# Performance work log

Measured on AMD Instinct MI355X. Metric: run time of the kernel, lower is better.

Reference implementation:

```python
import jax, jax.numpy as jnp
from jax import lax
import numpy as np

B, L = 256, 4096
H, RL, RH = 128, 2, 32   # num_hiddens, residual layers, residual hiddens
K, D = 512, 64           # codebook size, embedding dim
CC = 0.25                # commitment cost


def conv1d(x, w, b=None, stride=1, pad=0, circular=False):
    # x: (N,C,L), w: (O,I,k)
    if circular and pad > 0:
        x = jnp.pad(x, ((0, 0), (0, 0), (pad, pad)), mode='wrap')
        pad = 0
    y = lax.conv_general_dilated(x, w, (stride,), [(pad, pad)],
                                 dimension_numbers=('NCH', 'OIH', 'NCH'))
    return y if b is None else y + b[None, :, None]


def convt1d(x, w, b):
    # PyTorch ConvTranspose1d(k=4, s=2, p=1); w: (I,O,4). out_len = 2*L.
    wt = jnp.flip(jnp.swapaxes(w, 0, 1), -1)  # (O,I,4)
    y = lax.conv_general_dilated(x, wt, (1,), [(2, 2)], lhs_dilation=(2,),
                                 dimension_numbers=('NCH', 'OIH', 'NCH'))
    return y + b[None, :, None]


def res_stack(x, w1s, w2s):
    for i in range(w1s.shape[0]):
        h = conv1d(jax.nn.relu(x), w1s[i], None, 1, 1, circular=True)
        h = conv1d(jax.nn.relu(h), w2s[i], None, 1, 0)
        x = x + h
    return jax.nn.relu(x)


def setup_inputs() -> dict:
    key = jax.random.key(0)
    ks = iter(jax.random.split(key, 64))

    def w(*shape):
        fan_in = int(np.prod(shape[1:]))
        return jax.random.normal(next(ks), shape, jnp.float32) / np.sqrt(fan_in)

    def bias(n):
        return jax.random.uniform(next(ks), (n,), jnp.float32, -0.05, 0.05)

    inp = {'x': jax.random.normal(next(ks), (B, 1, L), jnp.float32)}
    # Encoder
    inp['enc_c1_w'] = w(H // 2, 1, 4);      inp['enc_c1_b'] = bias(H // 2)
    inp['enc_c2_w'] = w(H, H // 2, 4);      inp['enc_c2_b'] = bias(H)
    inp['enc_c3_w'] = w(H, H, 4);           inp['enc_c3_b'] = bias(H)
    inp['enc_c4_w'] = w(H, H, 4);           inp['enc_c4_b'] = bias(H)
    inp['enc_cf_w'] = w(H, H, 3);           inp['enc_cf_b'] = bias(H)
    inp['enc_res_w1'] = w(RL, RH, H, 3)
    inp['enc_res_w2'] = w(RL, H, RH, 1)
    # pre-VQ 1x1 conv
    inp['prevq_w'] = w(D, H, 1);            inp['prevq_b'] = bias(D)
    # codebook: uniform(-1/K, 1/K) as in source
    inp['emb'] = jax.random.uniform(next(ks), (K, D), jnp.float32, -1.0 / K, 1.0 / K)
    # Decoder
    inp['dec_init_w'] = w(H, D, 3);         inp['dec_init_b'] = bias(H)
    inp['dec_res_w1'] = w(RL, RH, H, 3)
    inp['dec_res_w2'] = w(RL, H, RH, 1)
    inp['ct0_w'] = w(H, H, 4);              inp['ct0_b'] = bias(H)
    inp['ct1_w'] = w(H, H, 4);              inp['ct1_b'] = bias(H)
    inp['ct2_w'] = w(H, H // 2, 4);         inp['ct2_b'] = bias(H // 2)
    inp['ct3_w'] = w(H // 2, 1, 4);         inp['ct3_b'] = bias(1)
    return inp


def _forward(x, enc_c1_w, enc_c1_b, enc_c2_w, enc_c2_b, enc_c3_w, enc_c3_b,
             enc_c4_w, enc_c4_b, enc_cf_w, enc_cf_b, enc_res_w1, enc_res_w2,
             prevq_w, prevq_b, emb, dec_init_w, dec_init_b, dec_res_w1,
             dec_res_w2, ct0_w, ct0_b, ct1_w, ct1_b, ct2_w, ct2_b, ct3_w, ct3_b):
    sg = lax.stop_gradient
    relu = jax.nn.relu
    # ---- Encoder (circular padding) ----
    z = relu(conv1d(x, enc_c1_w, enc_c1_b, 2, 1, circular=True))
    z = relu(conv1d(z, enc_c2_w, enc_c2_b, 2, 1, circular=True))
    z = relu(conv1d(z, enc_c3_w, enc_c3_b, 2, 1, circular=True))
    z = relu(conv1d(z, enc_c4_w, enc_c4_b, 2, 1, circular=True))
    z = conv1d(z, enc_cf_w, enc_cf_b, 1, 1, circular=True)
    z = res_stack(z, enc_res_w1, enc_res_w2)
    z = conv1d(z, prevq_w, prevq_b, 1, 0)        # (B, D, T)
    # ---- Vector quantizer ----
    z_t = jnp.transpose(z, (0, 2, 1))            # (B, T, D)
    flat = z_t.reshape(-1, D)                    # (BT, D)
    dist = (jnp.sum(flat ** 2, axis=1, keepdims=True)
            + jnp.sum(emb ** 2, axis=1)
            - 2.0 * flat @ emb.T)                # (BT, K)
    idx = jnp.argmin(dist, axis=1)               # (BT,)
    enc = jax.nn.one_hot(idx, K, dtype=flat.dtype)
    q = (enc @ emb).reshape(z_t.shape)           # (B, T, D)
    e_loss = jnp.mean((sg(q) - z_t) ** 2)
    q_loss = jnp.mean((q - sg(z_t)) ** 2)
    loss = q_loss + CC * e_loss
    q_st = z_t + sg(q - z_t)                     # straight-through
    avg = jnp.mean(enc, axis=0)
    perplexity = jnp.exp(-jnp.sum(avg * jnp.log(avg + 1e-10)))
    quantized = jnp.transpose(q_st, (0, 2, 1))   # (B, D, T)
    # ---- Decoder ----
    h = conv1d(quantized, dec_init_w, dec_init_b, 1, 1)
    h = res_stack(h, dec_res_w1, dec_res_w2)
    h = relu(convt1d(h, ct0_w, ct0_b))
    h = relu(convt1d(h, ct1_w, ct1_b))
    h = relu(convt1d(h, ct2_w, ct2_b))
    x_recon = convt1d(h, ct3_w, ct3_b)           # (B, 1, L)
    return loss, x_recon, perplexity


def reference(x, enc_c1_w, enc_c1_b, enc_c2_w, enc_c2_b, enc_c3_w, enc_c3_b,
              enc_c4_w, enc_c4_b, enc_cf_w, enc_cf_b, enc_res_w1, enc_res_w2,
              prevq_w, prevq_b, emb, dec_init_w, dec_init_b, dec_res_w1,
              dec_res_w2, ct0_w, ct0_b, ct1_w, ct1_b, ct2_w, ct2_b, ct3_w, ct3_b):
    return _forward(x, enc_c1_w, enc_c1_b, enc_c2_w, enc_c2_b, enc_c3_w,
                    enc_c3_b, enc_c4_w, enc_c4_b, enc_cf_w, enc_cf_b,
                    enc_res_w1, enc_res_w2, prevq_w, prevq_b, emb,
                    dec_init_w, dec_init_b, dec_res_w1, dec_res_w2,
                    ct0_w, ct0_b, ct1_w, ct1_b, ct2_w, ct2_b, ct3_w, ct3_b)
```

## Files before the change

### kernel.cpp

```cpp
#include <hip/hip_runtime.h>

#define DEVI __device__ __forceinline__

typedef __bf16 bf16x8 __attribute__((ext_vector_type(8)));
typedef float f32x4 __attribute__((ext_vector_type(4)));

DEVI ushort f2b(float f) {
  uint b = __float_as_uint(f);
  uint r = (b + 0x7FFFu + ((b >> 16) & 1u)) >> 16;
  return (ushort)r;
}
DEVI float b2f(ushort u) { return __uint_as_float(((uint)u) << 16); }

struct PrepArgs {
  int nw;
  int tot[20];
  const float* src[20];
  ushort* dst[20];
  int ci[20], co[20], sco[20], sci[20], sk[20];
};

__global__ __launch_bounds__(256)
void prep_all(PrepArgs a, int total) {
  int i = blockIdx.x * 256 + threadIdx.x;
  if (i >= total) return;
  int w = 0;
  while (i >= a.tot[w]) { i -= a.tot[w]; ++w; }
  const int li = i;
  const int CI = a.ci[w];
  int ciX = i % CI;
  int rest = i / CI;
  int coX = rest % a.co[w];
  int k = rest / a.co[w];
  a.dst[w][li] = f2b(a.src[w][coX * a.sco[w] + ciX * a.sci[w] + k * a.sk[w]]);
}

__global__ __launch_bounds__(256)
void enc1_bf(const float* __restrict__ x, const float* __restrict__ w1,
             const float* __restrict__ b1, ushort* __restrict__ out) {
  int i = blockIdx.x * 256 + threadIdx.x;
  int t = i & 2047, n = i >> 11;
  const float* xb = x + ((size_t)n << 12);
  int p = 2 * t - 1;
  float x0 = xb[(p + 4096) & 4095];
  float x1 = xb[(p + 4097) & 4095];
  float x2 = xb[(p + 4098) & 4095];
  float x3 = xb[(p + 4099) & 4095];
  uint ow[32];
  #pragma unroll
  for (int c2 = 0; c2 < 32; ++c2) {
    float4 wa = *reinterpret_cast<const float4*>(w1 + 8 * c2);
    float4 wb = *reinterpret_cast<const float4*>(w1 + 8 * c2 + 4);
    float s0 = fmaf(wa.x, x0, fmaf(wa.y, x1, fmaf(wa.z, x2, fmaf(wa.w, x3, b1[2 * c2]))));
    float s1 = fmaf(wb.x, x0, fmaf(wb.y, x1, fmaf(wb.z, x2, fmaf(wb.w, x3, b1[2 * c2 + 1]))));
    ow[c2] = (uint)f2b(fmaxf(s0, 0.0f)) | ((uint)f2b(fmaxf(s1, 0.0f)) << 16);
  }
  uint4* op = reinterpret_cast<uint4*>(out + ((size_t)i << 6));
  #pragma unroll
  for (int q = 0; q < 8; ++q)
    op[q] = uint4{ow[4 * q], ow[4 * q + 1], ow[4 * q + 2], ow[4 * q + 3]};
}

template<int CI, int CO, int K, int S, bool CIRC, bool GATHER, int NT, int WAVES_CO>
__global__ __launch_bounds__(256)
void conv_mfma(const ushort* __restrict__ in, const ushort* __restrict__ wb,
               const float* __restrict__ bias, const ushort* __restrict__ resid,
               ushort* __restrict__ out, const int* __restrict__ gidx,
               int Tin, int in_relu, int out_relu) {
  constexpr int PAD = (K > 1) ? 1 : 0;
  constexpr int TT = NT * 16;
  constexpr int SPAN = S * (TT - 1) + K;
  constexpr int CIG = CI / 8;
  constexpr int COT = CO / 16;
  constexpr int WCOT = COT / WAVES_CO;
  constexpr int WAVES_T = 4 / WAVES_CO;
  constexpr int WTT = NT / WAVES_T;
  constexpr int KSH = (S == 2) ? 1 : 0;
  static_assert(CI % 32 == 0 && COT % WAVES_CO == 0 && NT % WAVES_T == 0, "");

  __shared__ __align__(16) ushort xs[SPAN * CI];

  const int Tout = Tin / S;
  const int tilesPerB = Tout / TT;
  const int n = blockIdx.x / tilesPerB;
  const int t0 = (blockIdx.x % tilesPerB) * TT;
  const int tid = threadIdx.x;
  const int wid = tid >> 6, lane = tid & 63;
  const int l15 = lane & 15, l4 = lane >> 4;

  const int t_in0 = S * t0 - PAD;
  const ushort* inb = GATHER ? in : in + (size_t)n * Tin * CI;
  for (int i = tid; i < SPAN * CIG; i += 256) {
    int t = i / CIG, g = i - (i / CIG) * CIG;
    int tg = t_in0 + t;
    uint4 v;
    if (CIRC) {
      tg = (tg < 0) ? tg + Tin : (tg >= Tin ? tg - Tin : tg);
      v = *reinterpret_cast<const uint4*>(inb + (size_t)tg * CI + g * 8);
    } else if (GATHER) {
      if ((unsigned)tg < (unsigned)Tin) {
        int id = gidx[n * Tin + tg];
        v = *reinterpret_cast<const uint4*>(inb + (size_t)id * CI + g * 8);
      } else
        v = uint4{0, 0, 0, 0};
    } else {
      if ((unsigned)tg < (unsigned)Tin)
        v = *reinterpret_cast<const uint4*>(inb + (size_t)tg * CI + g * 8);
      else
        v = uint4{0, 0, 0, 0};
    }
    if (in_relu) {
      ushort* pv = reinterpret_cast<ushort*>(&v);
      #pragma unroll
      for (int e = 0; e < 8; ++e) pv[e] = (pv[e] & 0x8000) ? 0 : pv[e];
    }
    *reinterpret_cast<uint4*>(&xs[t * CI + ((g ^ ((t >> KSH) & (CIG - 1))) * 8)]) = v;
  }
  __syncthreads();

  const int wco = wid % WAVES_CO;
  const int wt = wid / WAVES_CO;
  const int co_base = wco * WCOT * 16;
  const int t_base = wt * WTT * 16;

  f32x4 acc[WTT][WCOT] = {};

  for (int cc = 0; cc < CI / 32; ++cc) {
    bf16x8 bk[K][WCOT];
    #pragma unroll
    for (int k = 0; k < K; ++k)
      #pragma unroll
      for (int c = 0; c < WCOT; ++c)
        bk[k][c] = __builtin_bit_cast(bf16x8, *reinterpret_cast<const uint4*>(
            wb + (size_t)((k * CO + co_base + c * 16 + l15)) * CI + cc * 32 + l4 * 8));
    #pragma unroll
    for (int k = 0; k < K; ++k) {
      #pragma unroll
      for (int tt2 = 0; tt2 < WTT; ++tt2) {
        int trow = S * (t_base + tt2 * 16 + l15) + k;
        int g = cc * 4 + l4;
        bf16x8 afr = __builtin_bit_cast(bf16x8, *reinterpret_cast<const uint4*>(
            &xs[trow * CI + ((g ^ ((trow >> KSH) & (CIG - 1))) * 8)]));
        #pragma unroll
        for (int c = 0; c < WCOT; ++c)
          acc[tt2][c] = __builtin_amdgcn_mfma_f32_16x16x32_bf16(afr, bk[k][c], acc[tt2][c], 0, 0, 0);
      }
    }
  }

  float bv[WCOT];
  #pragma unroll
  for (int c = 0; c < WCOT; ++c)
    bv[c] = bias ? bias[co_base + c * 16 + l15] : 0.0f;
  ushort* outb = out + (size_t)n * Tout * CO;
  const ushort* resb = resid ? resid + (size_t)n * Tout * CO : nullptr;
  #pragma unroll
  for (int tt2 = 0; tt2 < WTT; ++tt2)
    #pragma unroll
    for (int c = 0; c < WCOT; ++c)
      #pragma unroll
      for (int r = 0; r < 4; ++r) {
        int t = t0 + t_base + tt2 * 16 + 4 * l4 + r;
        int co = co_base + c * 16 + l15;
        float v = acc[tt2][c][r] + bv[c];
        if (resb) v += b2f(resb[(size_t)t * CO + co]);
        if (out_relu) v = fmaxf(v, 0.0f);
        outb[(size_t)t * CO + co] = f2b(v);
      }
}

__global__ __launch_bounds__(256)
void res_mfma(const ushort* __restrict__ in, const ushort* __restrict__ wb1,
              const ushort* __restrict__ wb2, ushort* __restrict__ out) {
  constexpr int CI = 128, CIG = 16;
  constexpr int TT = 64, SPAN = 66, Tin = 256;
  __shared__ __align__(16) ushort xs[SPAN * CI];
  __shared__ __align__(16) ushort hs[TT][40];
  const int n = blockIdx.x >> 2;
  const int t0 = (blockIdx.x & 3) * TT;
  const int tid = threadIdx.x;
  const int wid = tid >> 6, lane = tid & 63;
  const int l15 = lane & 15, l4 = lane >> 4;
  const int t_in0 = t0 - 1;
  const ushort* inb = in + (size_t)n * Tin * CI;

  for (int i = tid; i < SPAN * CIG; i += 256) {
    int t = i >> 4, g = i & 15;
    int tg = t_in0 + t;
    tg = (tg < 0) ? tg + Tin : (tg >= Tin ? tg - Tin : tg);
    uint4 v = *reinterpret_cast<const uint4*>(inb + (size_t)tg * CI + g * 8);
    ushort* pv = reinterpret_cast<ushort*>(&v);
    #pragma unroll
    for (int e = 0; e < 8; ++e) pv[e] = (pv[e] & 0x8000) ? 0 : pv[e];
    *reinterpret_cast<uint4*>(&xs[t * CI + ((g ^ (t & 15)) * 8)]) = v;
  }
  __syncthreads();

  {
    f32x4 acc[2] = {};
    for (int cc = 0; cc < 4; ++cc)
      #pragma unroll
      for (int k = 0; k < 3; ++k) {
        bf16x8 bfr[2];
        #pragma unroll
        for (int c = 0; c < 2; ++c)
          bfr[c] = __builtin_bit_cast(bf16x8, *reinterpret_cast<const uint4*>(
              wb1 + (size_t)((k * 32 + c * 16 + l15)) * CI + cc * 32 + l4 * 8));
        int trow = wid * 16 + l15 + k;
        int g = cc * 4 + l4;
        bf16x8 afr = __builtin_bit_cast(bf16x8, *reinterpret_cast<const uint4*>(
            &xs[trow * CI + ((g ^ (trow & 15)) * 8)]));
        acc[0] = __builtin_amdgcn_mfma_f32_16x16x32_bf16(afr, bfr[0], acc[0], 0, 0, 0);
        acc[1] = __builtin_amdgcn_mfma_f32_16x16x32_bf16(afr, bfr[1], acc[1], 0, 0, 0);
      }
    #pragma unroll
    for (int c = 0; c < 2; ++c)
      #pragma unroll
      for (int r = 0; r < 4; ++r) {
        float v = acc[c][r];
        hs[wid * 16 + l4 * 4 + r][c * 16 + l15] = (v > 0.0f) ? f2b(v) : (ushort)0;
      }
  }
  __syncthreads();

  {
    bf16x8 afr = *reinterpret_cast<const bf16x8*>(&hs[wid * 16 + l15][l4 * 8]);
    f32x4 acc[8];
    #pragma unroll
    for (int c = 0; c < 8; ++c) {
      bf16x8 bfr = __builtin_bit_cast(bf16x8, *reinterpret_cast<const uint4*>(
          wb2 + (size_t)(c * 16 + l15) * 32 + l4 * 8));
      f32x4 z = {};
      acc[c] = __builtin_amdgcn_mfma_f32_16x16x32_bf16(afr, bfr, z, 0, 0, 0);
    }
    ushort* outb = out + (size_t)n * Tin * CI;
    #pragma unroll
    for (int c = 0; c < 8; ++c)
      #pragma unroll
      for (int r = 0; r < 4; ++r) {
        int t = t0 + wid * 16 + l4 * 4 + r;
        int co = c * 16 + l15;
        float v = acc[c][r] + b2f(inb[(size_t)t * CI + co]);
        outb[(size_t)t * CI + co] = f2b(v);
      }
  }
}

template<int CO>
__global__ __launch_bounds__(256)
void convt_mfma(const ushort* __restrict__ in, const ushort* __restrict__ wb,
                const float* __restrict__ bias, ushort* __restrict__ out,
                int Tin, int in_relu, int out_relu) {
  constexpr int CI = 128, CIG = 16;
  constexpr int NT = 4, TT = 64;
  constexpr int SPAN = TT + 2;
  constexpr int COT = CO / 16;
  constexpr int WCOT = (COT + 3) / 4;
  constexpr int WAVES_CO = COT / WCOT;
  constexpr int WTT = NT;

  __shared__ __align__(16) ushort xs[SPAN * CI];

  const int Tout = 2 * Tin;
  const int tilesPerB = Tin / TT;
  const int n = blockIdx.x / tilesPerB;
  const int tp0 = (blockIdx.x % tilesPerB) * TT;
  const int tid = threadIdx.x;
  const int wid = tid >> 6, lane = tid & 63;
  const int l15 = lane & 15, l4 = lane >> 4;

  const int t_in0 = tp0 - 1;
  const ushort* inb = in + (size_t)n * Tin * CI;
  for (int i = tid; i < SPAN * CIG; i += 256) {
    int t = i >> 4, g = i & 15;
    int tg = t_in0 + t;
    uint4 v;
    if ((unsigned)tg < (unsigned)Tin)
      v = *reinterpret_cast<const uint4*>(inb + (size_t)tg * CI + g * 8);
    else
      v = uint4{0, 0, 0, 0};
    if (in_relu) {
      ushort* pv = reinterpret_cast<ushort*>(&v);
      #pragma unroll
      for (int e = 0; e < 8; ++e) pv[e] = (pv[e] & 0x8000) ? 0 : pv[e];
    }
    *reinterpret_cast<uint4*>(&xs[t * CI + ((g ^ (t & 15)) * 8)]) = v;
  }
  __syncthreads();

  const int wco = wid % WAVES_CO;
  const int co_base = wco * WCOT * 16;

  f32x4 accE[WTT][WCOT] = {};
  f32x4 accO[WTT][WCOT] = {};

  for (int cc = 0; cc < 4; ++cc) {
    bf16x8 bk[4][WCOT];
    #pragma unroll
    for (int k = 0; k < 4; ++k)
      #pragma unroll
      for (int c = 0; c < WCOT; ++c)
        bk[k][c] = __builtin_bit_cast(bf16x8, *reinterpret_cast<const uint4*>(
            wb + (size_t)((k * CO + co_base + c * 16 + l15)) * CI + cc * 32 + l4 * 8));
    #pragma unroll
    for (int tt2 = 0; tt2 < WTT; ++tt2) {
      int lt = tt2 * 16 + l15 + 1;
      int g = cc * 4 + l4;
      bf16x8 a0 = __builtin_bit_cast(bf16x8, *reinterpret_cast<const uint4*>(
          &xs[lt * CI + ((g ^ (lt & 15)) * 8)]));
      bf16x8 am = __builtin_bit_cast(bf16x8, *reinterpret_cast<const uint4*>(
          &xs[(lt - 1) * CI + ((g ^ ((lt - 1) & 15)) * 8)]));
      bf16x8 ap = __builtin_bit_cast(bf16x8, *reinterpret_cast<const uint4*>(
          &xs[(lt + 1) * CI + ((g ^ ((lt + 1) & 15)) * 8)]));
      #pragma unroll
      for (int c = 0; c < WCOT; ++c) {
        accE[tt2][c] = __builtin_amdgcn_mfma_f32_16x16x32_bf16(a0, bk[1][c], accE[tt2][c], 0, 0, 0);
        accE[tt2][c] = __builtin_amdgcn_mfma_f32_16x16x32_bf16(am, bk[3][c], accE[tt2][c], 0, 0, 0);
        accO[tt2][c] = __builtin_amdgcn_mfma_f32_16x16x32_bf16(ap, bk[0][c], accO[tt2][c], 0, 0, 0);
        accO[tt2][c] = __builtin_amdgcn_mfma_f32_16x16x32_bf16(a0, bk[2][c], accO[tt2][c], 0, 0, 0);
      }
    }
  }

  float bv[WCOT];
  #pragma unroll
  for (int c = 0; c < WCOT; ++c) bv[c] = bias[co_base + c * 16 + l15];
  ushort* outb = out + (size_t)n * Tout * CO;
  #pragma unroll
  for (int tt2 = 0; tt2 < WTT; ++tt2)
    #pragma unroll
    for (int c = 0; c < WCOT; ++c)
      #pragma unroll
      for (int r = 0; r < 4; ++r) {
        int tp = tp0 + tt2 * 16 + 4 * l4 + r;
        int co = co_base + c * 16 + l15;
        float vE = accE[tt2][c][r] + bv[c];
        float vO = accO[tt2][c][r] + bv[c];
        if (out_relu) { vE = fmaxf(vE, 0.0f); vO = fmaxf(vO, 0.0f); }
        outb[(size_t)(2 * tp) * CO + co] = f2b(vE);
        outb[(size_t)(2 * tp + 1) * CO + co] = f2b(vO);
      }
}

__global__ __launch_bounds__(256)
void ct23_mfma(const ushort* __restrict__ in, const ushort* __restrict__ wb,
               const float* __restrict__ bias, const float* __restrict__ w3,
               const float* __restrict__ b3, float* __restrict__ out) {
  constexpr int CI = 128, CO = 64, CIG = 16;
  constexpr int TT = 64, SPAN = 66, Tin = 1024;
  __shared__ __align__(16) ushort xs[SPAN * CI];
  __shared__ __align__(16) ushort ys[130 * 64];

  const int n = blockIdx.x >> 4;
  const int tp0 = (blockIdx.x & 15) * TT;
  const int tid = threadIdx.x;
  const int wid = tid >> 6, lane = tid & 63;
  const int l15 = lane & 15, l4 = lane >> 4;
  const int t_in0 = tp0 - 1;
  const ushort* inb = in + (size_t)n * Tin * CI;

  for (int i = tid; i < SPAN * CIG; i += 256) {
    int t = i >> 4, g = i & 15;
    int tg = t_in0 + t;
    uint4 v;
    if ((unsigned)tg < (unsigned)Tin)
      v = *reinterpret_cast<const uint4*>(inb + (size_t)tg * CI + g * 8);
    else
      v = uint4{0, 0, 0, 0};
    *reinterpret_cast<uint4*>(&xs[t * CI + ((g ^ (t & 15)) * 8)]) = v;
  }
  __syncthreads();

  const int co_base = wid * 16;
  f32x4 accE[4] = {}, accO[4] = {};
  f32x4 hO = {}, hE = {};

  for (int cc = 0; cc < 4; ++cc) {
    bf16x8 bk[4];
    #pragma unroll
    for (int k = 0; k < 4; ++k)
      bk[k] = __builtin_bit_cast(bf16x8, *reinterpret_cast<const uint4*>(
          wb + (size_t)((k * CO + co_base + l15)) * CI + cc * 32 + l4 * 8));
    const int g = cc * 4 + l4;
    auto rd = [&](int lt) -> bf16x8 {
      return __builtin_bit_cast(bf16x8, *reinterpret_cast<const uint4*>(
          &xs[lt * CI + ((g ^ (lt & 15)) * 8)]));
    };
    #pragma unroll
    for (int tt2 = 0; tt2 < 4; ++tt2) {
      int lt = tt2 * 16 + l15 + 1;
      bf16x8 a0 = rd(lt), am = rd(lt - 1), ap = rd(lt + 1);
      accE[tt2] = __builtin_amdgcn_mfma_f32_16x16x32_bf16(a0, bk[1], accE[tt2], 0, 0, 0);
      accE[tt2] = __builtin_amdgcn_mfma_f32_16x16x32_bf16(am, bk[3], accE[tt2], 0, 0, 0);
      accO[tt2] = __builtin_amdgcn_mfma_f32_16x16x32_bf16(ap, bk[0], accO[tt2], 0, 0, 0);
      accO[tt2] = __builtin_amdgcn_mfma_f32_16x16x32_bf16(a0, bk[2], accO[tt2], 0, 0, 0);
    }
    bf16x8 h0 = rd(0), h1 = rd(1), h64 = rd(64), h65 = rd(65);
    hO = __builtin_amdgcn_mfma_f32_16x16x32_bf16(h1, bk[0], hO, 0, 0, 0);
    hO = __builtin_amdgcn_mfma_f32_16x16x32_bf16(h0, bk[2], hO, 0, 0, 0);
    hE = __builtin_amdgcn_mfma_f32_16x16x32_bf16(h65, bk[1], hE, 0, 0, 0);
    hE = __builtin_amdgcn_mfma_f32_16x16x32_bf16(h64, bk[3], hE, 0, 0, 0);
  }

  const float bv = bias[co_base + l15];
  auto ywr = [&](int j, int co, float v) {
    int g = co >> 3, e = co & 7;
    ys[j * 64 + ((g ^ (j & 7)) * 8) + e] = f2b(fmaxf(v, 0.0f));
  };
  #pragma unroll
  for (int tt2 = 0; tt2 < 4; ++tt2)
    #pragma unroll
    for (int r = 0; r < 4; ++r) {
      int m = tt2 * 16 + 4 * l4 + r;
      ywr(2 * m + 1, co_base + l15, accE[tt2][r] + bv);
      ywr(2 * m + 2, co_base + l15, accO[tt2][r] + bv);
    }
  if (l4 == 0) {
    float vO = (tp0 == 0) ? -1.0f : hO[0] + bv;
    float vE = (tp0 + TT == Tin) ? -1.0f : hE[0] + bv;
    ywr(0, co_base + l15, vO);
    ywr(129, co_base + l15, vE);
  }
  __syncthreads();

  const int o = 4 * tp0 + tid;
  const int odd = o & 1;
  const int ga = odd ? ((o + 1) >> 1) : (o >> 1);
  const int gb = odd ? ((o - 1) >> 1) : (o / 2 - 1);
  const int ka = odd ? 0 : 1;
  const int kb = odd ? 2 : 3;
  const int la = ga - (2 * tp0 - 1), lb = gb - (2 * tp0 - 1);
  float s = b3[0];
  #pragma unroll
  for (int g = 0; g < 8; ++g) {
    uint4 va = *reinterpret_cast<const uint4*>(&ys[la * 64 + ((g ^ (la & 7)) * 8)]);
    uint4 vb = *reinterpret_cast<const uint4*>(&ys[lb * 64 + ((g ^ (lb & 7)) * 8)]);
    const ushort* pa = reinterpret_cast<const ushort*>(&va);
    const ushort* pb = reinterpret_cast<const ushort*>(&vb);
    #pragma unroll
    for (int e = 0; e < 8; ++e) {
      int ci = g * 8 + e;
      s = fmaf(w3[ci * 4 + ka], b2f(pa[e]), s);
      s = fmaf(w3[ci * 4 + kb], b2f(pb[e]), s);
    }
  }
  out[(size_t)n * 4096 + o] = s;
}

__global__ void ee_kernel(const float* __restrict__ emb, float* __restrict__ ee) {
  int c = blockIdx.x * 256 + threadIdx.x;
  if (c >= 512) return;
  float s = 0.0f;
  #pragma unroll
  for (int d = 0; d < 64; ++d) { float v = emb[c * 64 + d]; s = fmaf(v, v, s); }
  ee[c] = s;
}

__global__ __launch_bounds__(256)
void vq_mfma(const ushort* __restrict__ zt, const ushort* __restrict__ embb,
             const float* __restrict__ ee, int* __restrict__ idx,
             int* __restrict__ hist, float* __restrict__ loss_accum) {
  __shared__ __align__(16) ushort es[512 * 64];
  __shared__ float eel[512];
  __shared__ int lhist[512];
  const int tid = threadIdx.x;
  const int wid = tid >> 6, lane = tid & 63;
  const int l15 = lane & 15, l4 = lane >> 4;

  for (int i = tid; i < 512 * 8; i += 256) {
    int c = i >> 3, g = i & 7;
    reinterpret_cast<uint4*>(es)[c * 8 + (g ^ (c & 7))] =
        reinterpret_cast<const uint4*>(embb)[i];
  }
  for (int i = tid; i < 512; i += 256) { eel[i] = ee[i]; lhist[i] = 0; }
  __syncthreads();

  const int rb = blockIdx.x * 256 + wid * 64;
  bf16x8 bz[4][2];
  float zz[4], best[4];
  int bi[4];
  #pragma unroll
  for (int rt = 0; rt < 4; ++rt) {
    const int r = rb + rt * 16 + l15;
    uint4 v0 = *reinterpret_cast<const uint4*>(zt + (size_t)r * 64 + l4 * 8);
    uint4 v1 = *reinterpret_cast<const uint4*>(zt + (size_t)r * 64 + 32 + l4 * 8);
    bz[rt][0] = __builtin_bit_cast(bf16x8, v0);
    bz[rt][1] = __builtin_bit_cast(bf16x8, v1);
    float s = 0.0f;
    const ushort* p0 = reinterpret_cast<const ushort*>(&v0);
    const ushort* p1 = reinterpret_cast<const ushort*>(&v1);
    #pragma unroll
    for (int e = 0; e < 8; ++e) {
      float f0 = b2f(p0[e]), f1 = b2f(p1[e]);
      s = fmaf(f0, f0, fmaf(f1, f1, s));
    }
    s += __shfl_xor(s, 16);
    s += __shfl_xor(s, 32);
    zz[rt] = s;
    best[rt] = 3.4e38f;
    bi[rt] = 0;
  }

  for (int ct = 0; ct < 32; ++ct) {
    const int c = ct * 16 + l15;
    bf16x8 a0 = __builtin_bit_cast(bf16x8, reinterpret_cast<const uint4*>(es)[
        c * 8 + (l4 ^ (c & 7))]);
    bf16x8 a1 = __builtin_bit_cast(bf16x8, reinterpret_cast<const uint4*>(es)[
        c * 8 + ((4 | l4) ^ (c & 7))]);
    #pragma unroll
    for (int rt = 0; rt < 4; ++rt) {
      f32x4 acc = {};
      acc = __builtin_amdgcn_mfma_f32_16x16x32_bf16(a0, bz[rt][0], acc, 0, 0, 0);
      acc = __builtin_amdgcn_mfma_f32_16x16x32_bf16(a1, bz[rt][1], acc, 0, 0, 0);
      #pragma unroll
      for (int rr = 0; rr < 4; ++rr) {
        int code = ct * 16 + l4 * 4 + rr;
        float d = eel[code] - 2.0f * acc[rr];
        if (d < best[rt] || (d == best[rt] && code < bi[rt])) { best[rt] = d; bi[rt] = code; }
      }
    }
  }
  float vsum = 0.0f;
  #pragma unroll
  for (int rt = 0; rt < 4; ++rt) {
    #pragma unroll
    for (int m = 16; m <= 32; m <<= 1) {
      float ob = __shfl_xor(best[rt], m);
      int oi = __shfl_xor(bi[rt], m);
      if (ob < best[rt] || (ob == best[rt] && oi < bi[rt])) { best[rt] = ob; bi[rt] = oi; }
    }
    if (l4 == 0) {
      idx[rb + rt * 16 + l15] = bi[rt];
      atomicAdd(&lhist[bi[rt]], 1);
      vsum += zz[rt] + best[rt];
    }
  }
  #pragma unroll
  for (int m = 1; m < 64; m <<= 1) vsum += __shfl_xor(vsum, m);
  if (lane == 0) atomicAdd(loss_accum, vsum);
  __syncthreads();
  for (int i = tid; i < 512; i += 256)
    if (lhist[i]) atomicAdd(&hist[i], lhist[i]);
}

__global__ __launch_bounds__(512)
void finalize(const int* __restrict__ hist, const float* __restrict__ loss_accum,
              float* __restrict__ out) {
  __shared__ float red[8];
  int tid = threadIdx.x;
  float avg = (float)hist[tid] * (1.0f / 65536.0f);
  float v = avg * logf(avg + 1e-10f);
  for (int off = 32; off > 0; off >>= 1) v += __shfl_down(v, off);
  if ((tid & 63) == 0) red[tid >> 6] = v;
  __syncthreads();
  if (tid == 0) {
    float s = 0.0f;
    for (int i = 0; i < 8; ++i) s += red[i];
    out[1048577] = expf(-s);
    out[0] = 1.25f * loss_accum[0] * (1.0f / (65536.0f * 64.0f));
  }
}

extern "C" void kernel_launch(void* const* d_in, const int* in_sizes, int n_in,
                              void* d_out, int out_size, void* d_ws, size_t ws_size,
                              hipStream_t stream) {
  (void)in_sizes; (void)n_in; (void)out_size; (void)ws_size;
  const float* x    = (const float*)d_in[0];
  const float* c1w  = (const float*)d_in[1];
  const float* c1b  = (const float*)d_in[2];
  const float* c2w  = (const float*)d_in[3];
  const float* c2b  = (const float*)d_in[4];
  const float* c3w  = (const float*)d_in[5];
  const float* c3b  = (const float*)d_in[6];
  const float* c4w  = (const float*)d_in[7];
  const float* c4b  = (const float*)d_in[8];
  const float* cfw  = (const float*)d_in[9];
  const float* cfb  = (const float*)d_in[10];
  const float* erw1 = (const float*)d_in[11];
  const float* erw2 = (const float*)d_in[12];
  const float* pqw  = (const float*)d_in[13];
  const float* pqb  = (const float*)d_in[14];
  const float* emb  = (const float*)d_in[15];
  const float* diw  = (const float*)d_in[16];
  const float* dib  = (const float*)d_in[17];
  const float* drw1 = (const float*)d_in[18];
  const float* drw2 = (const float*)d_in[19];
  const float* t0w  = (const float*)d_in[20];
  const float* t0b  = (const float*)d_in[21];
  const float* t1w  = (const float*)d_in[22];
  const float* t1b  = (const float*)d_in[23];
  const float* t2w  = (const float*)d_in[24];
  const float* t2b  = (const float*)d_in[25];
  const float* t3w  = (const float*)d_in[26];
  const float* t3b  = (const float*)d_in[27];

  char* wsb = (char*)d_ws;
  ushort* R0 = (ushort*)wsb;
  ushort* R1 = (ushort*)(wsb + 67108864);
  ushort* R2 = (ushort*)(wsb + 134217728);
  ushort* R3 = (ushort*)(wsb + 0);
  ushort* R4 = (ushort*)(wsb + 16777216);
  ushort* R6 = (ushort*)(wsb + 37748736);
  ushort* WPu = (ushort*)(wsb + 167772160);
  ushort* wb_e2 = WPu + 0;
  ushort* wb_e3 = WPu + 32768;
  ushort* wb_e4 = WPu + 98304;
  ushort* wb_cf = WPu + 163840;
  ushort* wb_r1a = WPu + 212992;
  ushort* wb_r1b = WPu + 225280;
  ushort* wb_r2a = WPu + 237568;
  ushort* wb_r2b = WPu + 241664;
  ushort* wb_pq = WPu + 245760;
  ushort* wb_di = WPu + 253952;
  ushort* wb_d1a = WPu + 278528;
  ushort* wb_d1b = WPu + 290816;
  ushort* wb_d2a = WPu + 303104;
  ushort* wb_d2b = WPu + 307200;
  ushort* wb_t0 = WPu + 311296;
  ushort* wb_t1 = WPu + 376832;
  ushort* wb_t2 = WPu + 442368;
  ushort* wb_emb = WPu + 475136;
  char* fp = wsb + 167772160 + 1048576;
  float* eeb   = (float*)fp;
  int*   idxb  = (int*)(fp + 2048);
  int*   histb = (int*)(fp + 2048 + 262144);
  float* lossb = (float*)(fp + 2048 + 262144 + 2048);
  float* outp  = (float*)d_out;

  hipMemsetAsync(histb, 0, 512 * sizeof(int), stream);
  hipMemsetAsync(lossb, 0, sizeof(float), stream);

  PrepArgs pa{};
  int nw = 0, total = 0;
  auto addw = [&](const float* src, ushort* dst, int CO, int CI, int K,
                  int sco, int sci, int sk) {
    pa.tot[nw] = K * CO * CI; pa.src[nw] = src; pa.dst[nw] = dst;
    pa.ci[nw] = CI; pa.co[nw] = CO; pa.sco[nw] = sco; pa.sci[nw] = sci; pa.sk[nw] = sk;
    total += pa.tot[nw]; ++nw;
  };
  addw(c2w, wb_e2, 128, 64, 4, 256, 4, 1);
  addw(c3w, wb_e3, 128, 128, 4, 512, 4, 1);
  addw(c4w, wb_e4, 128, 128, 4, 512, 4, 1);
  addw(cfw, wb_cf, 128, 128, 3, 384, 3, 1);
  addw(erw1, wb_r1a, 32, 128, 3, 384, 3, 1);
  addw(erw1 + 12288, wb_r1b, 32, 128, 3, 384, 3, 1);
  addw(erw2, wb_r2a, 128, 32, 1, 32, 1, 1);
  addw(erw2 + 4096, wb_r2b, 128, 32, 1, 32, 1, 1);
  addw(pqw, wb_pq, 64, 128, 1, 128, 1, 1);
  addw(diw, wb_di, 128, 64, 3, 192, 3, 1);
  addw(drw1, wb_d1a, 32, 128, 3, 384, 3, 1);
  addw(drw1 + 12288, wb_d1b, 32, 128, 3, 384, 3, 1);
  addw(drw2, wb_d2a, 128, 32, 1, 32, 1, 1);
  addw(drw2 + 4096, wb_d2b, 128, 32, 1, 32, 1, 1);
  addw(t0w, wb_t0, 128, 128, 4, 4, 512, 1);
  addw(t1w, wb_t1, 128, 128, 4, 4, 512, 1);
  addw(t2w, wb_t2, 64, 128, 4, 4, 256, 1);
  addw(emb, wb_emb, 512, 64, 1, 64, 1, 1);
  pa.nw = nw;
  prep_all<<<(total + 255) / 256, 256, 0, stream>>>(pa, total);
  ee_kernel<<<2, 256, 0, stream>>>(emb, eeb);

  enc1_bf<<<2048, 256, 0, stream>>>(x, c1w, c1b, R0);
  conv_mfma<64, 128, 4, 2, true, false, 4, 4><<<4096, 256, 0, stream>>>(R0, wb_e2, c2b, nullptr, R1, nullptr, 2048, 0, 1);
  conv_mfma<128, 128, 4, 2, true, false, 4, 4><<<2048, 256, 0, stream>>>(R1, wb_e3, c3b, nullptr, R2, nullptr, 1024, 0, 1);
  conv_mfma<128, 128, 4, 2, true, false, 4, 4><<<1024, 256, 0, stream>>>(R2, wb_e4, c4b, nullptr, R3, nullptr, 512, 0, 1);
  conv_mfma<128, 128, 3, 1, true, false, 8, 2><<<512, 256, 0, stream>>>(R3, wb_cf, cfb, nullptr, R4, nullptr, 256, 0, 0);
  res_mfma<<<1024, 256, 0, stream>>>(R4, wb_r1a, wb_r2a, R3);
  res_mfma<<<1024, 256, 0, stream>>>(R3, wb_r1b, wb_r2b, R4);
  conv_mfma<128, 64, 1, 1, false, false, 8, 2><<<512, 256, 0, stream>>>(R4, wb_pq, pqb, nullptr, R6, nullptr, 256, 1, 0);
  vq_mfma<<<256, 256, 0, stream>>>(R6, wb_emb, eeb, idxb, histb, lossb);
  finalize<<<1, 512, 0, stream>>>(histb, lossb, outp);
  conv_mfma<64, 128, 3, 1, false, true, 8, 2><<<512, 256, 0, stream>>>(wb_emb, wb_di, dib, nullptr, R3, idxb, 256, 0, 0);
  res_mfma<<<1024, 256, 0, stream>>>(R3, wb_d1a, wb_d2a, R4);
  res_mfma<<<1024, 256, 0, stream>>>(R4, wb_d1b, wb_d2b, R3);
  convt_mfma<128><<<1024, 256, 0, stream>>>(R3, wb_t0, t0b, R2, 256, 1, 1);
  convt_mfma<128><<<2048, 256, 0, stream>>>(R2, wb_t1, t1b, R0, 512, 0, 1);
  ct23_mfma<<<4096, 256, 0, stream>>>(R0, wb_t2, t2b, t3w, t3b, outp + 1);
}
```

Before: 458.5 us.

## Split enc1 across channel octets, restage ct23 LDS, fold codebook norms into VQ

The first encoder conv now gives each thread 8 output channels instead of 64, using 8x more threads so each thread writes one coalesced 16-byte store. In ct23, the intermediate is stored in LDS channel-major with padded rows, and the final 64-to-1 transposed conv reads scalar LDS entries against weights cached in LDS instead of global memory. The separate ee_kernel launch is removed, and codebook squared norms are computed inside vq_mfma from the bf16 codebook. That norm now uses bf16-rounded values rather than fp32, which may change argmin ties slightly.

```diff
diff --git a/kernel.cpp b/kernel.cpp
--- a/kernel.cpp
+++ b/kernel.cpp
@@ -39,26 +39,26 @@
 void enc1_bf(const float* __restrict__ x, const float* __restrict__ w1,
              const float* __restrict__ b1, ushort* __restrict__ out) {
   int i = blockIdx.x * 256 + threadIdx.x;
-  int t = i & 2047, n = i >> 11;
+  int oct = i & 7;
+  int t = (i >> 3) & 2047;
+  int n = i >> 14;
   const float* xb = x + ((size_t)n << 12);
   int p = 2 * t - 1;
   float x0 = xb[(p + 4096) & 4095];
   float x1 = xb[(p + 4097) & 4095];
   float x2 = xb[(p + 4098) & 4095];
   float x3 = xb[(p + 4099) & 4095];
-  uint ow[32];
-  #pragma unroll
-  for (int c2 = 0; c2 < 32; ++c2) {
-    float4 wa = *reinterpret_cast<const float4*>(w1 + 8 * c2);
-    float4 wb = *reinterpret_cast<const float4*>(w1 + 8 * c2 + 4);
-    float s0 = fmaf(wa.x, x0, fmaf(wa.y, x1, fmaf(wa.z, x2, fmaf(wa.w, x3, b1[2 * c2]))));
-    float s1 = fmaf(wb.x, x0, fmaf(wb.y, x1, fmaf(wb.z, x2, fmaf(wb.w, x3, b1[2 * c2 + 1]))));
-    ow[c2] = (uint)f2b(fmaxf(s0, 0.0f)) | ((uint)f2b(fmaxf(s1, 0.0f)) << 16);
-  }
-  uint4* op = reinterpret_cast<uint4*>(out + ((size_t)i << 6));
-  #pragma unroll
-  for (int q = 0; q < 8; ++q)
-    op[q] = uint4{ow[4 * q], ow[4 * q + 1], ow[4 * q + 2], ow[4 * q + 3]};
+  uint pack[4];
+  #pragma unroll
+  for (int h = 0; h < 4; ++h) {
+    int c0 = oct * 8 + 2 * h;
+    float4 wa = *reinterpret_cast<const float4*>(w1 + 4 * c0);
+    float4 wc = *reinterpret_cast<const float4*>(w1 + 4 * c0 + 4);
+    float s0 = fmaf(wa.x, x0, fmaf(wa.y, x1, fmaf(wa.z, x2, fmaf(wa.w, x3, b1[c0]))));
+    float s1 = fmaf(wc.x, x0, fmaf(wc.y, x1, fmaf(wc.z, x2, fmaf(wc.w, x3, b1[c0 + 1]))));
+    pack[h] = (uint)f2b(fmaxf(s0, 0.0f)) | ((uint)f2b(fmaxf(s1, 0.0f)) << 16);
+  }
+  *reinterpret_cast<uint4*>(out + (size_t)i * 8) = uint4{pack[0], pack[1], pack[2], pack[3]};
 }
 
 template<int CI, int CO, int K, int S, bool CIRC, bool GATHER, int NT, int WAVES_CO>
@@ -349,7 +349,8 @@
   constexpr int CI = 128, CO = 64, CIG = 16;
   constexpr int TT = 64, SPAN = 66, Tin = 1024;
   __shared__ __align__(16) ushort xs[SPAN * CI];
-  __shared__ __align__(16) ushort ys[130 * 64];
+  __shared__ ushort ys[64 * 134];
+  __shared__ float w3s[256];
 
   const int n = blockIdx.x >> 4;
   const int tp0 = (blockIdx.x & 15) * TT;
@@ -359,6 +360,7 @@
   const int t_in0 = tp0 - 1;
   const ushort* inb = in + (size_t)n * Tin * CI;
 
+  if (tid < 256) w3s[tid] = w3[tid];
   for (int i = tid; i < SPAN * CIG; i += 256) {
     int t = i >> 4, g = i & 15;
     int tg = t_in0 + t;
@@ -403,23 +405,18 @@
   }
 
   const float bv = bias[co_base + l15];
-  auto ywr = [&](int j, int co, float v) {
-    int g = co >> 3, e = co & 7;
-    ys[j * 64 + ((g ^ (j & 7)) * 8) + e] = f2b(fmaxf(v, 0.0f));
-  };
+  ushort* yrow = &ys[(co_base + l15) * 134];
   #pragma unroll
   for (int tt2 = 0; tt2 < 4; ++tt2)
     #pragma unroll
     for (int r = 0; r < 4; ++r) {
       int m = tt2 * 16 + 4 * l4 + r;
-      ywr(2 * m + 1, co_base + l15, accE[tt2][r] + bv);
-      ywr(2 * m + 2, co_base + l15, accO[tt2][r] + bv);
+      yrow[2 * m + 1] = f2b(fmaxf(accE[tt2][r] + bv, 0.0f));
+      yrow[2 * m + 2] = f2b(fmaxf(accO[tt2][r] + bv, 0.0f));
     }
   if (l4 == 0) {
-    float vO = (tp0 == 0) ? -1.0f : hO[0] + bv;
-    float vE = (tp0 + TT == Tin) ? -1.0f : hE[0] + bv;
-    ywr(0, co_base + l15, vO);
-    ywr(129, co_base + l15, vE);
+    yrow[0]   = (tp0 == 0) ? (ushort)0 : f2b(fmaxf(hO[0] + bv, 0.0f));
+    yrow[129] = (tp0 + TT == Tin) ? (ushort)0 : f2b(fmaxf(hE[0] + bv, 0.0f));
   }
   __syncthreads();
 
@@ -429,37 +426,20 @@
   const int gb = odd ? ((o - 1) >> 1) : (o / 2 - 1);
   const int ka = odd ? 0 : 1;
   const int kb = odd ? 2 : 3;
-  const int la = ga - (2 * tp0 - 1), lb = gb - (2 * tp0 - 1);
+  const int ja = ga - (2 * tp0 - 1), jb = gb - (2 * tp0 - 1);
   float s = b3[0];
-  #pragma unroll
-  for (int g = 0; g < 8; ++g) {
-    uint4 va = *reinterpret_cast<const uint4*>(&ys[la * 64 + ((g ^ (la & 7)) * 8)]);
-    uint4 vb = *reinterpret_cast<const uint4*>(&ys[lb * 64 + ((g ^ (lb & 7)) * 8)]);
-    const ushort* pa = reinterpret_cast<const ushort*>(&va);
-    const ushort* pb = reinterpret_cast<const ushort*>(&vb);
-    #pragma unroll
-    for (int e = 0; e < 8; ++e) {
-      int ci = g * 8 + e;
-      s = fmaf(w3[ci * 4 + ka], b2f(pa[e]), s);
-      s = fmaf(w3[ci * 4 + kb], b2f(pb[e]), s);
-    }
+  #pragma unroll 16
+  for (int ci = 0; ci < 64; ++ci) {
+    s = fmaf(w3s[ci * 4 + ka], b2f(ys[ci * 134 + ja]), s);
+    s = fmaf(w3s[ci * 4 + kb], b2f(ys[ci * 134 + jb]), s);
   }
   out[(size_t)n * 4096 + o] = s;
-}
-
-__global__ void ee_kernel(const float* __restrict__ emb, float* __restrict__ ee) {
-  int c = blockIdx.x * 256 + threadIdx.x;
-  if (c >= 512) return;
-  float s = 0.0f;
-  #pragma unroll
-  for (int d = 0; d < 64; ++d) { float v = emb[c * 64 + d]; s = fmaf(v, v, s); }
-  ee[c] = s;
 }
 
 __global__ __launch_bounds__(256)
 void vq_mfma(const ushort* __restrict__ zt, const ushort* __restrict__ embb,
-             const float* __restrict__ ee, int* __restrict__ idx,
-             int* __restrict__ hist, float* __restrict__ loss_accum) {
+             int* __restrict__ idx, int* __restrict__ hist,
+             float* __restrict__ loss_accum) {
   __shared__ __align__(16) ushort es[512 * 64];
   __shared__ float eel[512];
   __shared__ int lhist[512];
@@ -469,10 +449,18 @@
 
   for (int i = tid; i < 512 * 8; i += 256) {
     int c = i >> 3, g = i & 7;
-    reinterpret_cast<uint4*>(es)[c * 8 + (g ^ (c & 7))] =
-        reinterpret_cast<const uint4*>(embb)[i];
-  }
-  for (int i = tid; i < 512; i += 256) { eel[i] = ee[i]; lhist[i] = 0; }
+    uint4 v = reinterpret_cast<const uint4*>(embb)[i];
+    reinterpret_cast<uint4*>(es)[c * 8 + (g ^ (c & 7))] = v;
+    const ushort* pv = reinterpret_cast<const ushort*>(&v);
+    float ss = 0.0f;
+    #pragma unroll
+    for (int e = 0; e < 8; ++e) { float f = b2f(pv[e]); ss = fmaf(f, f, ss); }
+    ss += __shfl_xor(ss, 1);
+    ss += __shfl_xor(ss, 2);
+    ss += __shfl_xor(ss, 4);
+    if ((i & 7) == 0) eel[c] = ss;
+  }
+  for (int i = tid; i < 512; i += 256) lhist[i] = 0;
   __syncthreads();
 
   const int rb = blockIdx.x * 256 + wid * 64;
@@ -621,7 +609,6 @@
   ushort* wb_t2 = WPu + 442368;
   ushort* wb_emb = WPu + 475136;
   char* fp = wsb + 167772160 + 1048576;
-  float* eeb   = (float*)fp;
   int*   idxb  = (int*)(fp + 2048);
   int*   histb = (int*)(fp + 2048 + 262144);
   float* lossb = (float*)(fp + 2048 + 262144 + 2048);
@@ -658,9 +645,8 @@
   addw(emb, wb_emb, 512, 64, 1, 64, 1, 1);
   pa.nw = nw;
   prep_all<<<(total + 255) / 256, 256, 0, stream>>>(pa, total);
-  ee_kernel<<<2, 256, 0, stream>>>(emb, eeb);
-
-  enc1_bf<<<2048, 256, 0, stream>>>(x, c1w, c1b, R0);
+
+  enc1_bf<<<16384, 256, 0, stream>>>(x, c1w, c1b, R0);
   conv_mfma<64, 128, 4, 2, true, false, 4, 4><<<4096, 256, 0, stream>>>(R0, wb_e2, c2b, nullptr, R1, nullptr, 2048, 0, 1);
   conv_mfma<128, 128, 4, 2, true, false, 4, 4><<<2048, 256, 0, stream>>>(R1, wb_e3, c3b, nullptr, R2, nullptr, 1024, 0, 1);
   conv_mfma<128, 128, 4, 2, true, false, 4, 4><<<1024, 256, 0, stream>>>(R2, wb_e4, c4b, nullptr, R3, nullptr, 512, 0, 1);
@@ -668,7 +654,7 @@
   res_mfma<<<1024, 256, 0, stream>>>(R4, wb_r1a, wb_r2a, R3);
   res_mfma<<<1024, 256, 0, stream>>>(R3, wb_r1b, wb_r2b, R4);
   conv_mfma<128, 64, 1, 1, false, false, 8, 2><<<512, 256, 0, stream>>>(R4, wb_pq, pqb, nullptr, R6, nullptr, 256, 1, 0);
-  vq_mfma<<<256, 256, 0, stream>>>(R6, wb_emb, eeb, idxb, histb, lossb);
+  vq_mfma<<<256, 256, 0, stream>>>(R6, wb_emb, idxb, histb, lossb);
   finalize<<<1, 512, 0, stream>>>(histb, lossb, outp);
   conv_mfma<64, 128, 3, 1, false, true, 8, 2><<<512, 256, 0, stream>>>(wb_emb, wb_di, dib, nullptr, R3, idxb, 256, 0, 0);
   res_mfma<<<1024, 256, 0, stream>>>(R3, wb_d1a, wb_d2a, R4);
```

Result: slower. 498.0 us (+8.6%).
